# Kernel optimization log

Hardware: AMD Instinct MI355X
Metric: run time of the kernel (lower is better)

## Reference

```python
import jax, jax.numpy as jnp
import numpy as np

N_EMBD = 1024
N_HEAD = 16


def setup_inputs() -> dict:
    key = jax.random.key(0)
    k1, k2, k3, k4, k5 = jax.random.split(key, 5)
    B, T, C = 4, 2048, N_EMBD
    s = 1.0 / np.sqrt(C)
    x = jax.random.normal(k1, (B, T, C), dtype=jnp.float32)
    w_weight = jax.random.normal(k2, (3 * C, C), dtype=jnp.float32) * s
    w_bias = jax.random.normal(k3, (3 * C,), dtype=jnp.float32) * s
    proj_weight = jax.random.normal(k4, (C, C), dtype=jnp.float32) * s
    proj_bias = jax.random.normal(k5, (C,), dtype=jnp.float32) * s
    return {"x": x, "w_weight": w_weight, "w_bias": w_bias,
            "proj_weight": proj_weight, "proj_bias": proj_bias}


def reference(x, w_weight, w_bias, proj_weight, proj_bias):
    B, T, C = x.shape
    nh = N_HEAD
    hs = C // nh
    # fused QKV projection (torch Linear: x @ W^T + b)
    wei = jnp.einsum('btc,oc->bto', x, w_weight) + w_bias
    k, q, v = jnp.split(wei, 3, axis=-1)  # note: chunk order is k, q, v
    # [B, T, nh, hs] -> [B, nh, T, hs]
    key_ = k.reshape(B, T, nh, hs).transpose(0, 2, 1, 3)
    query = q.reshape(B, T, nh, hs).transpose(0, 2, 1, 3)
    value = v.reshape(B, T, nh, hs).transpose(0, 2, 1, 3)
    scale = hs ** (-0.5)
    weight = jnp.einsum('bhqd,bhkd->bhqk', query, key_) * scale
    weight = jax.nn.softmax(weight, axis=-1)
    out = jnp.einsum('bhqk,bhkd->bhqd', weight, value)  # [B, nh, T, hs]
    # Faithful to source bug: transpose(1,2) is discarded; view is taken on
    # the (B, nh, T, hs) layout directly.
    out = out.reshape(B, T, C)
    out = jnp.einsum('btc,oc->bto', out, proj_weight) + proj_bias
    return out
```

## Files before the change

### kernel.cpp

```cpp
#include <hip/hip_runtime.h>
#include <hip/hip_bf16.h>


typedef __attribute__((ext_vector_type(8)))  short bf16x8;
typedef __attribute__((ext_vector_type(4)))  float f32x4;
typedef __attribute__((ext_vector_type(16))) float f32x16;
typedef __attribute__((ext_vector_type(2)))  unsigned u32x2;

typedef __attribute__((address_space(3))) unsigned lds_u32_t;
typedef __attribute__((address_space(1))) unsigned glb_u32_t;

__device__ __forceinline__ void async_cp16(const short* g, short* l) {
    __builtin_amdgcn_global_load_lds((glb_u32_t*)g, (lds_u32_t*)l, 16, 0, 0);
}

__device__ __forceinline__ float exp2fast(float x) {
    return __builtin_amdgcn_exp2f(x);
}

__device__ __forceinline__ short f2bf(float f) {
    union { float f; unsigned u; } v; v.f = f;
    unsigned r = v.u + 0x7fffu + ((v.u >> 16) & 1u);
    return (short)(r >> 16);
}

__device__ __forceinline__ unsigned cvt_pk_bf16(float lo, float hi) {
    unsigned r;
    asm("v_cvt_pk_bf16_f32 %0, %1, %2" : "=v"(r) : "v"(lo), "v"(hi));
    return r;
}

__global__ __launch_bounds__(256) void cvt3_kernel(
    const float4* __restrict__ x,  const float4* __restrict__ ww,
    const float4* __restrict__ pw, short4* __restrict__ xb,
    short4* __restrict__ wwb,      short4* __restrict__ pwb) {
    const int b = blockIdx.x;
    const float4* in; short4* out; int i;
    if (b < 8192)       { in = x;  out = xb;  i = b * 256 + threadIdx.x; }
    else if (b < 11264) { in = ww; out = wwb; i = (b - 8192) * 256 + threadIdx.x; }
    else                { in = pw; out = pwb; i = (b - 11264) * 256 + threadIdx.x; }
    float4 v = in[i];
    short4 o;
    o.x = f2bf(v.x); o.y = f2bf(v.y); o.z = f2bf(v.z); o.w = f2bf(v.w);
    out[i] = o;
}

template<int EPI>
__global__ __launch_bounds__(256) void gemm_bf16(
    const short* __restrict__ A, const short* __restrict__ W,
    const float* __restrict__ bias, float* __restrict__ outF,
    short* __restrict__ kout, short* __restrict__ qout, short* __restrict__ vtout,
    int M, int N, int K)
{
    __shared__ short lA[2][128 * 64];
    __shared__ short lB[2][128 * 64];
    const int tid  = threadIdx.x;
    const int lane = tid & 63;
    const int wave = tid >> 6;
    const int wM = (wave >> 1) * 64;
    const int wN = (wave & 1) * 64;
    const int l15 = lane & 15, l4 = lane >> 4;
    const int rsw = (lane & 7) << 3;

    const int lin = blockIdx.y * gridDim.x + blockIdx.x;
    const int byp = 8 * (lin & 7) + ((lin >> 3) & 7);
    const int bxp = lin >> 6;
    const int rowBase = byp * 128;
    const int colBase = bxp * 128;

    auto STAGE = [&](int t, int buf) {
        const int k0 = t * 64;
        #pragma unroll
        for (int i = 0; i < 4; ++i) {
            int idx = i * 256 + tid;
            int r   = idx >> 3;
            int cp  = ((idx & 7) ^ (r & 7)) * 8;
            int eo  = idx * 8;
            async_cp16(A + (size_t)(rowBase + r) * K + k0 + cp, &lA[buf][eo]);
            async_cp16(W + (size_t)(colBase + r) * K + k0 + cp, &lB[buf][eo]);
        }
    };

    f32x4 acc[4][4] = {};
    const int NT = K >> 6;

    STAGE(0, 0);
    __syncthreads();

    int cur = 0;
    for (int t = 0; t < NT; ++t) {
        if (t + 1 < NT) STAGE(t + 1, cur ^ 1);
        #pragma unroll
        for (int kt = 0; kt < 2; ++kt) {
            bf16x8 af[4], bfr[4];
            #pragma unroll
            for (int mt = 0; mt < 4; ++mt)
                af[mt] = *(const bf16x8*)(
                    &lA[cur][(wM + mt * 16 + l15) * 64 + ((kt * 32 + l4 * 8) ^ rsw)]);
            #pragma unroll
            for (int nt = 0; nt < 4; ++nt)
                bfr[nt] = *(const bf16x8*)(
                    &lB[cur][(wN + nt * 16 + l15) * 64 + ((kt * 32 + l4 * 8) ^ rsw)]);
            #pragma unroll
            for (int mt = 0; mt < 4; ++mt)
                #pragma unroll
                for (int nt = 0; nt < 4; ++nt)
                    acc[mt][nt] = __builtin_amdgcn_mfma_f32_16x16x32_bf16(
                        af[mt], bfr[nt], acc[mt][nt], 0, 0, 0);
        }
        __syncthreads();
        cur ^= 1;
    }

    #pragma unroll
    for (int mt = 0; mt < 4; ++mt) {
        #pragma unroll
        for (int nt = 0; nt < 4; ++nt) {
            const int n  = colBase + wN + nt * 16 + l15;
            const int mb = rowBase + wM + mt * 16 + l4 * 4;
            const float bv = bias[n];
            #pragma unroll
            for (int r = 0; r < 4; ++r) {
                const int m = mb + r;
                float val = acc[mt][nt][r] + bv;
                if (EPI == 0) {
                    int b = m >> 11, t = m & 2047;
                    int j = n >> 10, hd = n & 1023;
                    int h = hd >> 6, d = hd & 63;
                    size_t base = ((size_t)(b * 16 + h) * 2048 + t) * 64 + d;
                    if (j == 0)      kout[base] = f2bf(val);
                    else if (j == 1) qout[base] = f2bf(val * 0.180336879f);
                    else             vtout[((size_t)(b * 16 + h) * 64 + d) * 2048 + t] = f2bf(val);
                } else {
                    outF[(size_t)m * N + n] = val;
                }
            }
        }
    }
}

__global__ __launch_bounds__(256) void attn_kernel(
    const short* __restrict__ Q, const short* __restrict__ Km,
    const short* __restrict__ Vt, short* __restrict__ O)
{
    __shared__ short kbuf[2][64 * 64];
    __shared__ short vbuf[2][64 * 64];

    const int tid  = threadIdx.x;
    const int lane = tid & 63;
    const int wave = tid >> 6;
    const int l31 = lane & 31;
    const int l1  = lane >> 5;

    const int b     = blockIdx.x;
    const int xcd   = b & 7;
    const int inner = b >> 3;
    const int bx    = inner & 15;
    const int bh    = xcd * 8 + (inner >> 4);
    const int q0    = bx * 128 + wave * 32;

    const short* Qh = Q  + (size_t)bh * 2048 * 64;
    const short* Kh = Km + (size_t)bh * 2048 * 64;
    const short* Vh = Vt + (size_t)bh * 64 * 2048;

    const int i8 = lane >> 3, i7 = lane & 7;
    const int srcCol = 8 * (i7 ^ i8);
    const int rsw    = (l31 & 7) << 3;

    const short* src[4];
    short* dst0[4];
    int step;
    if (wave < 2) {
        #pragma unroll
        for (int c = 0; c < 4; ++c) {
            int j = wave * 4 + c;
            src[c]  = Kh + (size_t)(8 * j + i8) * 64 + srcCol;
            dst0[c] = &kbuf[0][j * 512 + lane * 8];
        }
        step = 64 * 64;
    } else {
        #pragma unroll
        for (int c = 0; c < 4; ++c) {
            int j = (wave - 2) * 4 + c;
            src[c]  = Vh + (size_t)(8 * j + i8) * 2048 + srcCol;
            dst0[c] = &vbuf[0][j * 512 + lane * 8];
        }
        step = 64;
    }
    auto STAGE_K = [&](int buf) {
        if (wave < 2) {
            #pragma unroll
            for (int c = 0; c < 4; ++c) {
                async_cp16(src[c], dst0[c] + buf * 4096);
                src[c] += step;
            }
        }
    };
    auto STAGE_V = [&](int buf) {
        if (wave >= 2) {
            #pragma unroll
            for (int c = 0; c < 4; ++c) {
                async_cp16(src[c], dst0[c] + buf * 4096);
                src[c] += step;
            }
        }
    };

    bf16x8 qf[4];
    #pragma unroll
    for (int s = 0; s < 4; ++s)
        qf[s] = *(const bf16x8*)(Qh + (size_t)(q0 + l31) * 64 + s * 16 + l1 * 8);

    union { unsigned u[4]; bf16x8 v; } onesu;
    #pragma unroll
    for (int j = 0; j < 4; ++j) onesu.u[j] = 0x3F803F80u;
    const bf16x8 onesf = onesu.v;

    f32x16 o[2] = {};
    f32x16 ol   = {};
    f32x16 s2a[2], s2b[2];

    auto QK = [&](int kb, f32x16* out) {
        f32x16 r0 = {}, r1 = {};
        __builtin_amdgcn_s_setprio(1);
        #pragma unroll
        for (int s = 0; s < 4; ++s) {
            bf16x8 kf0 = *(const bf16x8*)(
                &kbuf[kb][(l31) * 64 + ((s * 16 + l1 * 8) ^ rsw)]);
            r0 = __builtin_amdgcn_mfma_f32_32x32x16_bf16(kf0, qf[s], r0, 0, 0, 0);
            bf16x8 kf1 = *(const bf16x8*)(
                &kbuf[kb][(32 + l31) * 64 + ((s * 16 + l1 * 8) ^ rsw)]);
            r1 = __builtin_amdgcn_mfma_f32_32x32x16_bf16(kf1, qf[s], r1, 0, 0, 0);
        }
        __builtin_amdgcn_s_setprio(0);
        out[0] = r0; out[1] = r1;
    };

    auto SMPV = [&](f32x16* s2, int vb) {
        #pragma unroll
        for (int t = 0; t < 2; ++t)
            #pragma unroll
            for (int i = 0; i < 16; ++i)
                s2[t][i] = exp2fast(s2[t][i]);
        bf16x8 pa[4];
        #pragma unroll
        for (int t = 0; t < 2; ++t) {
            #pragma unroll
            for (int sl = 0; sl < 2; ++sl) {
                unsigned A0 = cvt_pk_bf16(s2[t][8 * sl + 0], s2[t][8 * sl + 1]);
                unsigned A1 = cvt_pk_bf16(s2[t][8 * sl + 2], s2[t][8 * sl + 3]);
                unsigned B0 = cvt_pk_bf16(s2[t][8 * sl + 4], s2[t][8 * sl + 5]);
                unsigned B1 = cvt_pk_bf16(s2[t][8 * sl + 6], s2[t][8 * sl + 7]);
                u32x2 ra = __builtin_amdgcn_permlane32_swap(A0, B0, false, false);
                u32x2 rb = __builtin_amdgcn_permlane32_swap(A1, B1, false, false);
                union { unsigned u[4]; bf16x8 v; } w;
                w.u[0] = ra.x;
                w.u[1] = rb.x;
                w.u[2] = ra.y;
                w.u[3] = rb.y;
                pa[2 * t + sl] = w.v;
            }
        }
        __builtin_amdgcn_s_setprio(1);
        #pragma unroll
        for (int s = 0; s < 4; ++s) {
            #pragma unroll
            for (int dt = 0; dt < 2; ++dt) {
                bf16x8 vf = *(const bf16x8*)(
                    &vbuf[vb][(dt * 32 + l31) * 64 + ((s * 16 + l1 * 8) ^ rsw)]);
                o[dt] = __builtin_amdgcn_mfma_f32_32x32x16_bf16(pa[s], vf, o[dt], 0, 0, 0);
            }
            ol = __builtin_amdgcn_mfma_f32_32x32x16_bf16(pa[s], onesf, ol, 0, 0, 0);
        }
        __builtin_amdgcn_s_setprio(0);
    };

    STAGE_K(0);
    __syncthreads();
    STAGE_K(1);
    STAGE_V(0);
    QK(0, s2a);
    __syncthreads();
    for (int i = 0; i < 15; ++i) {
        STAGE_K(0);
        STAGE_V(1);
        QK(1, s2b);
        SMPV(s2a, 0);
        __syncthreads();
        STAGE_K(1);
        STAGE_V(0);
        QK(0, s2a);
        SMPV(s2b, 1);
        __syncthreads();
    }
    STAGE_V(1);
    QK(1, s2b);
    SMPV(s2a, 0);
    __syncthreads();
    SMPV(s2b, 1);

    #pragma unroll
    for (int g = 0; g < 4; ++g)
        #pragma unroll
        for (int rr = 0; rr < 4; ++rr) {
            float invl = 1.f / ol[g * 4 + rr];
            int qrow = q0 + rr + 8 * g + 4 * l1;
            size_t base = ((size_t)bh * 2048 + qrow) * 64 + l31;
            O[base]      = f2bf(o[0][g * 4 + rr] * invl);
            O[base + 32] = f2bf(o[1][g * 4 + rr] * invl);
        }
}

extern "C" void kernel_launch(void* const* d_in, const int* in_sizes, int n_in,
                              void* d_out, int out_size, void* d_ws, size_t ws_size,
                              hipStream_t stream) {
    const float* x  = (const float*)d_in[0];
    const float* ww = (const float*)d_in[1];
    const float* wb = (const float*)d_in[2];
    const float* pwt = (const float*)d_in[3];
    const float* pb  = (const float*)d_in[4];
    float* out = (float*)d_out;

    short* ws  = (short*)d_ws;
    short* xb  = ws;
    short* wwb = xb  + 8192 * 1024;
    short* pwb = wwb + 3072 * 1024;
    short* qb  = pwb + 1024 * 1024;
    short* kb  = qb  + 64 * 2048 * 64;
    short* vtb = kb  + 64 * 2048 * 64;
    short* ob  = vtb + 64 * 2048 * 64;

    cvt3_kernel<<<12288, 256, 0, stream>>>(
        (const float4*)x, (const float4*)ww, (const float4*)pwt,
        (short4*)xb, (short4*)wwb, (short4*)pwb);

    gemm_bf16<0><<<dim3(24, 64), 256, 0, stream>>>(
        xb, wwb, wb, nullptr, kb, qb, vtb, 8192, 3072, 1024);

    attn_kernel<<<1024, 256, 0, stream>>>(qb, kb, vtb, ob);

    gemm_bf16<1><<<dim3(8, 64), 256, 0, stream>>>(
        ob, pwb, pb, out, nullptr, nullptr, nullptr, 8192, 1024, 1024);
}
```

Measured before the change: 198.7 us.

## Load V fragments directly from global into registers, bypassing LDS

The attention kernel no longer stages V tiles through shared memory. Each wave loads its V MFMA operands straight from global memory into registers per key block, and all four waves now share the K staging. This removes the V LDS traffic and halves the shared-memory footprint. In exchange every wave re-reads the same V tile from global/L2, which adds memory traffic and exposes load latency that the LDS double-buffer used to hide.

```diff
diff --git a/kernel.cpp b/kernel.cpp
--- a/kernel.cpp
+++ b/kernel.cpp
@@ -144,7 +144,6 @@
     const short* __restrict__ Vt, short* __restrict__ O)
 {
     __shared__ short kbuf[2][64 * 64];
-    __shared__ short vbuf[2][64 * 64];
 
     const int tid  = threadIdx.x;
     const int lane = tid & 63;
@@ -163,47 +162,32 @@
     const short* Kh = Km + (size_t)bh * 2048 * 64;
     const short* Vh = Vt + (size_t)bh * 64 * 2048;
 
-    const int i8 = lane >> 3, i7 = lane & 7;
-    const int srcCol = 8 * (i7 ^ i8);
-    const int rsw    = (l31 & 7) << 3;
-
-    const short* src[4];
-    short* dst0[4];
-    int step;
-    if (wave < 2) {
-        #pragma unroll
-        for (int c = 0; c < 4; ++c) {
-            int j = wave * 4 + c;
-            src[c]  = Kh + (size_t)(8 * j + i8) * 64 + srcCol;
-            dst0[c] = &kbuf[0][j * 512 + lane * 8];
-        }
-        step = 64 * 64;
-    } else {
-        #pragma unroll
-        for (int c = 0; c < 4; ++c) {
-            int j = (wave - 2) * 4 + c;
-            src[c]  = Vh + (size_t)(8 * j + i8) * 2048 + srcCol;
-            dst0[c] = &vbuf[0][j * 512 + lane * 8];
-        }
-        step = 64;
-    }
+    const int rsw = (l31 & 7) << 3;
+
+    const int krow0 = 16 * wave + (lane >> 3);
+    const int scol  = 8 * ((lane & 7) ^ (lane >> 3));
+    const short* ksrc0 = Kh + (size_t)krow0 * 64 + scol;
+    const short* ksrc1 = ksrc0 + 8 * 64;
+    short* kdst0 = &kbuf[0][wave * 1024 + lane * 8];
+    short* kdst1 = kdst0 + 512;
     auto STAGE_K = [&](int buf) {
-        if (wave < 2) {
-            #pragma unroll
-            for (int c = 0; c < 4; ++c) {
-                async_cp16(src[c], dst0[c] + buf * 4096);
-                src[c] += step;
-            }
-        }
-    };
-    auto STAGE_V = [&](int buf) {
-        if (wave >= 2) {
-            #pragma unroll
-            for (int c = 0; c < 4; ++c) {
-                async_cp16(src[c], dst0[c] + buf * 4096);
-                src[c] += step;
-            }
-        }
+        async_cp16(ksrc0, kdst0 + buf * 4096);
+        async_cp16(ksrc1, kdst1 + buf * 4096);
+        ksrc0 += 64 * 64;
+        ksrc1 += 64 * 64;
+    };
+
+    const short* vsrc0 = Vh + (size_t)l31 * 2048 + l1 * 8;
+    const short* vsrc1 = Vh + (size_t)(32 + l31) * 2048 + l1 * 8;
+    bf16x8 vf[4][2];
+    auto VLOAD = [&]() {
+        #pragma unroll
+        for (int s = 0; s < 4; ++s) {
+            vf[s][0] = *(const bf16x8*)(vsrc0 + s * 16);
+            vf[s][1] = *(const bf16x8*)(vsrc1 + s * 16);
+        }
+        vsrc0 += 64;
+        vsrc1 += 64;
     };
 
     bf16x8 qf[4];
@@ -221,22 +205,22 @@
     f32x16 s2a[2], s2b[2];
 
     auto QK = [&](int kb, f32x16* out) {
-        f32x16 r0 = {}, r1 = {};
+        f32x16 r0v = {}, r1v = {};
         __builtin_amdgcn_s_setprio(1);
         #pragma unroll
         for (int s = 0; s < 4; ++s) {
             bf16x8 kf0 = *(const bf16x8*)(
                 &kbuf[kb][(l31) * 64 + ((s * 16 + l1 * 8) ^ rsw)]);
-            r0 = __builtin_amdgcn_mfma_f32_32x32x16_bf16(kf0, qf[s], r0, 0, 0, 0);
+            r0v = __builtin_amdgcn_mfma_f32_32x32x16_bf16(kf0, qf[s], r0v, 0, 0, 0);
             bf16x8 kf1 = *(const bf16x8*)(
                 &kbuf[kb][(32 + l31) * 64 + ((s * 16 + l1 * 8) ^ rsw)]);
-            r1 = __builtin_amdgcn_mfma_f32_32x32x16_bf16(kf1, qf[s], r1, 0, 0, 0);
+            r1v = __builtin_amdgcn_mfma_f32_32x32x16_bf16(kf1, qf[s], r1v, 0, 0, 0);
         }
         __builtin_amdgcn_s_setprio(0);
-        out[0] = r0; out[1] = r1;
-    };
-
-    auto SMPV = [&](f32x16* s2, int vb) {
+        out[0] = r0v; out[1] = r1v;
+    };
+
+    auto SMPV = [&](f32x16* s2) {
         #pragma unroll
         for (int t = 0; t < 2; ++t)
             #pragma unroll
@@ -265,11 +249,8 @@
         #pragma unroll
         for (int s = 0; s < 4; ++s) {
             #pragma unroll
-            for (int dt = 0; dt < 2; ++dt) {
-                bf16x8 vf = *(const bf16x8*)(
-                    &vbuf[vb][(dt * 32 + l31) * 64 + ((s * 16 + l1 * 8) ^ rsw)]);
-                o[dt] = __builtin_amdgcn_mfma_f32_32x32x16_bf16(pa[s], vf, o[dt], 0, 0, 0);
-            }
+            for (int dt = 0; dt < 2; ++dt)
+                o[dt] = __builtin_amdgcn_mfma_f32_32x32x16_bf16(pa[s], vf[s][dt], o[dt], 0, 0, 0);
             ol = __builtin_amdgcn_mfma_f32_32x32x16_bf16(pa[s], onesf, ol, 0, 0, 0);
         }
         __builtin_amdgcn_s_setprio(0);
@@ -278,26 +259,25 @@
     STAGE_K(0);
     __syncthreads();
     STAGE_K(1);
-    STAGE_V(0);
     QK(0, s2a);
     __syncthreads();
     for (int i = 0; i < 15; ++i) {
+        VLOAD();
         STAGE_K(0);
-        STAGE_V(1);
         QK(1, s2b);
-        SMPV(s2a, 0);
+        SMPV(s2a);
         __syncthreads();
+        VLOAD();
         STAGE_K(1);
-        STAGE_V(0);
         QK(0, s2a);
-        SMPV(s2b, 1);
+        SMPV(s2b);
         __syncthreads();
     }
-    STAGE_V(1);
+    VLOAD();
     QK(1, s2b);
-    SMPV(s2a, 0);
-    __syncthreads();
-    SMPV(s2b, 1);
+    SMPV(s2a);
+    VLOAD();
+    SMPV(s2b);
 
     #pragma unroll
     for (int g = 0; g < 4; ++g)
```

New measurement: 298.7 us. +50.3%, slower.
